# Kernel tuning notes

Measured on AMD Instinct MI355X. Metric: run time of the kernel, lower is better.

Reference implementation:

```python
import jax, jax.numpy as jnp
import numpy as np

B, S, D, H = 4, 2048, 1024, 16
HD = D // H


def sinusoidal_pe(max_len, d_model):
    pos = np.arange(max_len)[:, None].astype(np.float32)
    div = np.exp(np.arange(0, d_model, 2).astype(np.float32) * (-np.log(10000.0) / d_model))
    pe = np.zeros((max_len, d_model), dtype=np.float32)
    pe[:, 0::2] = np.sin(pos * div)
    pe[:, 1::2] = np.cos(pos * div)
    return jnp.asarray(pe)


def setup_inputs() -> dict:
    key = jax.random.key(0)
    ks = jax.random.split(key, 9)
    s = 1.0 / np.sqrt(D)
    inp = {
        "x": jax.random.normal(ks[0], (B, S, D), dtype=jnp.float32),
        "Wq": jax.random.normal(ks[1], (D, D), dtype=jnp.float32) * s,
        "bq": jnp.zeros((D,), dtype=jnp.float32),
        "Wk": jax.random.normal(ks[2], (D, D), dtype=jnp.float32) * s,
        "bk": jnp.zeros((D,), dtype=jnp.float32),
        "Wv": jax.random.normal(ks[3], (D, D), dtype=jnp.float32) * s,
        "bv": jnp.zeros((D,), dtype=jnp.float32),
        "Wp": jax.random.normal(ks[4], (D, D), dtype=jnp.float32) * s,
        "bp": jnp.zeros((D,), dtype=jnp.float32),
        "pe": sinusoidal_pe(S, D),
    }
    return inp


def reference(x, Wq, bq, Wk, bk, Wv, bv, Wp, bp, pe):
    # positional encoding (eval mode: dropout is identity)
    xp = x + pe[None, :, :]  # [B,S,D]
    split = lambda t: t.reshape(B, S, H, HD).transpose(0, 2, 1, 3)  # [B,H,S,HD]
    q = split(xp @ Wq.T + bq)
    k = split(xp @ Wk.T + bk)
    v = split(xp @ Wv.T + bv)
    scores = jnp.einsum("bhqd,bhkd->bhqk", q, k) / jnp.sqrt(jnp.float32(HD))
    attn = jax.nn.softmax(scores, axis=-1)
    ctx = jnp.einsum("bhqk,bhkd->bhqd", attn, v)
    ctx = ctx.transpose(0, 2, 1, 3).reshape(B, S, D)
    return ctx @ Wp.T + bp
```

## Files before the change

### kernel.cpp

```cpp
#include <hip/hip_runtime.h>
#include <hip/hip_bf16.h>
#include <stdint.h>

#define B_  4
#define S_  2048
#define D_  1024
#define H_  16
#define HD_ 64

typedef __bf16 bfx8   __attribute__((ext_vector_type(8)));
typedef float  f32x4  __attribute__((ext_vector_type(4)));
typedef float  f32x16 __attribute__((ext_vector_type(16)));
typedef short  s16x4  __attribute__((ext_vector_type(4)));
typedef float  fl4    __attribute__((ext_vector_type(4)));
typedef unsigned int u32x2 __attribute__((ext_vector_type(2)));
typedef unsigned int u32x4 __attribute__((ext_vector_type(4)));

#define EXP2(x) __builtin_amdgcn_exp2f(x)

static __device__ __forceinline__ unsigned short f2bf(float f) {
    union { float f; unsigned int u; } v; v.f = f;
    unsigned int r = v.u + 0x7fffu + ((v.u >> 16) & 1u);
    return (unsigned short)(r >> 16);
}
static __device__ __forceinline__ unsigned int fbits(float f) {
    union { float f; unsigned int u; } v; v.f = f; return v.u;
}

#define GLD_LDS16(gp, lp) __builtin_amdgcn_global_load_lds( \
    (const __attribute__((address_space(1))) unsigned int*)(gp), \
    (__attribute__((address_space(3))) unsigned int*)(lp), 16, 0, 0)

__global__ __launch_bounds__(256) void prep_kernel(
    const float* __restrict__ x, const float* __restrict__ pe,
    const float* __restrict__ w0, const float* __restrict__ w1,
    const float* __restrict__ w2, const float* __restrict__ w3,
    unsigned short* __restrict__ xpb, unsigned short* __restrict__ wcat)
{
    const int blk = blockIdx.x;
    if (blk < 8192) {
        int i = (blk * 256 + threadIdx.x) * 4;
        fl4 xv = *(const fl4*)(x + i);
        fl4 pv = *(const fl4*)(pe + (i & (S_ * D_ - 1)));
        s16x4 r;
#pragma unroll
        for (int j = 0; j < 4; j++) r[j] = (short)f2bf(xv[j] + pv[j]);
        *(s16x4*)(xpb + i) = r;
    } else {
        const int bb = blk - 8192;
        const int wsel = bb >> 10;
        const float* src = wsel == 0 ? w0 : wsel == 1 ? w1 : wsel == 2 ? w2 : w3;
        int i = (((bb & 1023) * 256) + threadIdx.x) * 4;
        fl4 v = *(const fl4*)(src + i);
        s16x4 r;
#pragma unroll
        for (int j = 0; j < 4; j++) r[j] = (short)f2bf(v[j]);
        *(s16x4*)(wcat + (size_t)wsel * D_ * D_ + i) = r;
    }
}

__global__ __launch_bounds__(256, 3) void gemm_qkv(
    const unsigned short* __restrict__ A,
    const unsigned short* __restrict__ Bw,
    const float* __restrict__ bq, const float* __restrict__ bk,
    const float* __restrict__ bv,
    unsigned short* __restrict__ Qo, unsigned short* __restrict__ Ko,
    unsigned short* __restrict__ Vo, float qscale)
{
    constexpr int K = D_;
    __shared__ unsigned short As[2][128 * 32];
    __shared__ unsigned short Bs[2][128 * 32];
    const int hw  = blockIdx.x;
    const int xcd = hw & 7;
    const int i_  = hw >> 3;
    const int m0  = (i_ / 3) * 128;
    const int n0  = (xcd * 3 + i_ % 3) * 128;

    const int t  = threadIdx.x;
    const int l  = t & 63;
    const int w  = t >> 6;
    const int wr = (w >> 1) * 64;
    const int wc = (w & 1) * 64;
    const int lr = l & 15;
    const int lg = l >> 4;
    const int lk = lg * 8;

    const int e0 = t * 8;
    const int sr = e0 >> 5;
    const int sc = e0 & 31;
    const unsigned short* pA = A  + (size_t)(m0 + sr) * K + sc;
    const unsigned short* pB = Bw + (size_t)(n0 + sr) * K + sc;

    f32x4 acc[4][4] = {};

    GLD_LDS16(pA,                    As[0] + e0);
    GLD_LDS16(pA + (size_t)64 * K,   As[0] + 2048 + e0);
    GLD_LDS16(pB,                    Bs[0] + e0);
    GLD_LDS16(pB + (size_t)64 * K,   Bs[0] + 2048 + e0);
    __syncthreads();

    int cur = 0;
    for (int k0 = 0; k0 < K; k0 += 32) {
        if (k0 + 32 < K) {
            GLD_LDS16(pA + k0 + 32,                    As[cur ^ 1] + e0);
            GLD_LDS16(pA + k0 + 32 + (size_t)64 * K,   As[cur ^ 1] + 2048 + e0);
            GLD_LDS16(pB + k0 + 32,                    Bs[cur ^ 1] + e0);
            GLD_LDS16(pB + k0 + 32 + (size_t)64 * K,   Bs[cur ^ 1] + 2048 + e0);
        }
        const unsigned short* Ac = As[cur];
        const unsigned short* Bc = Bs[cur];
        bfx8 af[4], bf[4];
#pragma unroll
        for (int i = 0; i < 4; i++)
            af[i] = *(const bfx8*)(Ac + (wr + i * 16 + lr) * 32 + lk);
#pragma unroll
        for (int i = 0; i < 4; i++)
            bf[i] = *(const bfx8*)(Bc + (wc + i * 16 + lr) * 32 + lk);
#pragma unroll
        for (int i = 0; i < 4; i++)
#pragma unroll
            for (int j = 0; j < 4; j++)
                acc[i][j] = __builtin_amdgcn_mfma_f32_16x16x32_bf16(
                    af[i], bf[j], acc[i][j], 0, 0, 0);
        __syncthreads();
        cur ^= 1;
    }

    const int sel = n0 >> 10;
    const float* bias = sel == 0 ? bq : sel == 1 ? bk : bv;
    const float osc = sel == 0 ? qscale : 1.0f;

#pragma unroll
    for (int i = 0; i < 4; i++) {
        const int row0 = m0 + wr + i * 16 + lg * 4;
#pragma unroll
        for (int j = 0; j < 4; j++) {
            const int colf = n0 + wc + j * 16 + lr;
            const int ocol = colf & 1023;
            const float bvv = bias[ocol];
            if (sel < 2) {
                unsigned short* C = sel == 0 ? Qo : Ko;
#pragma unroll
                for (int v = 0; v < 4; v++)
                    C[(size_t)(row0 + v) * D_ + ocol] = f2bf((acc[i][j][v] + bvv) * osc);
            } else {
                const int bidx = row0 >> 11;
                const int s0   = row0 & (S_ - 1);
                s16x4 r;
#pragma unroll
                for (int v = 0; v < 4; v++) r[v] = (short)f2bf(acc[i][j][v] + bvv);
                *(s16x4*)(Vo + (size_t)(bidx * D_ + ocol) * S_ + s0) = r;
            }
        }
    }
}

__global__ __launch_bounds__(256, 3) void gemm_out(
    const unsigned short* __restrict__ A,
    const unsigned short* __restrict__ Bw,
    const float* __restrict__ bias,
    float* __restrict__ Cout)
{
    constexpr int K = D_;
    constexpr int N = D_;
    __shared__ unsigned short As[2][128 * 32];
    __shared__ unsigned short Bs[2][128 * 32];
    const int hw = blockIdx.x;
    const int logical = (hw & 7) * 64 + (hw >> 3);
    const int m0 = (logical >> 3) * 128;
    const int n0 = (logical & 7) * 128;

    const int t  = threadIdx.x;
    const int l  = t & 63;
    const int w  = t >> 6;
    const int wr = (w >> 1) * 64;
    const int wc = (w & 1) * 64;
    const int lr = l & 15;
    const int lg = l >> 4;
    const int lk = lg * 8;

    const int e0 = t * 8;
    const int sr = e0 >> 5;
    const int sc = e0 & 31;
    const unsigned short* pA = A  + (size_t)(m0 + sr) * K + sc;
    const unsigned short* pB = Bw + (size_t)(n0 + sr) * K + sc;

    f32x4 acc[4][4] = {};

    GLD_LDS16(pA,                    As[0] + e0);
    GLD_LDS16(pA + (size_t)64 * K,   As[0] + 2048 + e0);
    GLD_LDS16(pB,                    Bs[0] + e0);
    GLD_LDS16(pB + (size_t)64 * K,   Bs[0] + 2048 + e0);
    __syncthreads();

    int cur = 0;
    for (int k0 = 0; k0 < K; k0 += 32) {
        if (k0 + 32 < K) {
            GLD_LDS16(pA + k0 + 32,                    As[cur ^ 1] + e0);
            GLD_LDS16(pA + k0 + 32 + (size_t)64 * K,   As[cur ^ 1] + 2048 + e0);
            GLD_LDS16(pB + k0 + 32,                    Bs[cur ^ 1] + e0);
            GLD_LDS16(pB + k0 + 32 + (size_t)64 * K,   Bs[cur ^ 1] + 2048 + e0);
        }
        const unsigned short* Ac = As[cur];
        const unsigned short* Bc = Bs[cur];
        bfx8 af[4], bf[4];
#pragma unroll
        for (int i = 0; i < 4; i++)
            af[i] = *(const bfx8*)(Ac + (wr + i * 16 + lr) * 32 + lk);
#pragma unroll
        for (int i = 0; i < 4; i++)
            bf[i] = *(const bfx8*)(Bc + (wc + i * 16 + lr) * 32 + lk);
#pragma unroll
        for (int i = 0; i < 4; i++)
#pragma unroll
            for (int j = 0; j < 4; j++)
                acc[i][j] = __builtin_amdgcn_mfma_f32_16x16x32_bf16(
                    af[i], bf[j], acc[i][j], 0, 0, 0);
        __syncthreads();
        cur ^= 1;
    }

#pragma unroll
    for (int i = 0; i < 4; i++) {
        const int row0 = m0 + wr + i * 16 + lg * 4;
#pragma unroll
        for (int j = 0; j < 4; j++) {
            const int col = n0 + wc + j * 16 + lr;
            const float bv = bias[col];
#pragma unroll
            for (int v = 0; v < 4; v++)
                Cout[(size_t)(row0 + v) * N + col] = acc[i][j][v] + bv;
        }
    }
}

__global__ __launch_bounds__(256, 4) void attn_kernel(
    const unsigned short* __restrict__ Qb,
    const unsigned short* __restrict__ Kb,
    const unsigned short* __restrict__ Vt,
    unsigned short* __restrict__ Ctx)
{
    __shared__ __align__(16) unsigned short Ks[2][32 * 128];
    __shared__ __align__(16) unsigned short Vs[2][32 * 128];

    const int hw = blockIdx.x;
    const int logical = (hw & 7) * 128 + (hw >> 3);
    const int bh = logical >> 4;
    const int t  = threadIdx.x;
    const int l  = t & 63;
    const int w  = t >> 6;
    const int b  = bh >> 4;
    const int h  = bh & 15;
    const int lr = l & 31;
    const int hi = l >> 5;
    const int q0 = (logical & 15) * 128 + w * 32;

    const unsigned short* Qbase = Qb + (size_t)b * S_ * D_ + h * HD_;
    const unsigned short* Kbase = Kb + (size_t)b * S_ * D_ + h * HD_;
    const unsigned short* Vbase = Vt + (size_t)bh * HD_ * S_;

    const int jrow = t >> 4;
    const int c16  = (t & 15) ^ jrow;
    const int r0   = jrow + 32 * (c16 >> 3);
    const int cc8  = (c16 & 7) * 8;
    const unsigned short* Ksrc0 = Kbase + (size_t)r0 * D_ + cc8;
    const unsigned short* Ksrc1 = Kbase + (size_t)(r0 + 16) * D_ + cc8;
    const unsigned short* Vsrc0 = Vbase + (size_t)r0 * S_ + cc8;
    const unsigned short* Vsrc1 = Vbase + (size_t)(r0 + 16) * S_ + cc8;
    const int ld0 = t * 8, ld1 = t * 8 + 2048;

    GLD_LDS16(Ksrc0, &Ks[0][ld0]);
    GLD_LDS16(Ksrc1, &Ks[0][ld1]);
    GLD_LDS16(Vsrc0, &Vs[0][ld0]);
    GLD_LDS16(Vsrc1, &Vs[0][ld1]);

    bfx8 qf[4];
#pragma unroll
    for (int t4 = 0; t4 < 4; t4++)
        qf[t4] = *(const bfx8*)(Qbase + (size_t)(q0 + lr) * D_ + t4 * 16 + hi * 8);

    f32x16 acc0 = {}, acc1 = {};
    float l_r = 0.f;
    const int sw16 = lr & 15;

#define FRD(buf, half, cs) \
    (*(const bfx8*)((buf) + lr * 128 + ((((half) * 8 + (cs)) ^ sw16) * 8)))

    int cur = 0;
    for (int ki = 0; ki < S_ / 64; ki++) {
        __syncthreads();
        if (ki + 1 < S_ / 64) {
            GLD_LDS16(Ksrc0 + (size_t)(ki + 1) * 64 * D_, &Ks[cur ^ 1][ld0]);
            GLD_LDS16(Ksrc1 + (size_t)(ki + 1) * 64 * D_, &Ks[cur ^ 1][ld1]);
            GLD_LDS16(Vsrc0 + (ki + 1) * 64,              &Vs[cur ^ 1][ld0]);
            GLD_LDS16(Vsrc1 + (ki + 1) * 64,              &Vs[cur ^ 1][ld1]);
        }
        const unsigned short* Kc = Ks[cur];
        const unsigned short* Vc = Vs[cur];

        f32x16 s0 = {}, s1 = {};
        __builtin_amdgcn_s_setprio(1);
#pragma unroll
        for (int t4 = 0; t4 < 4; t4++) {
            bfx8 a0 = FRD(Kc, 0, t4 * 2 + hi);
            bfx8 a1 = FRD(Kc, 1, t4 * 2 + hi);
            s0 = __builtin_amdgcn_mfma_f32_32x32x16_bf16(a0, qf[t4], s0, 0, 0, 0);
            s1 = __builtin_amdgcn_mfma_f32_32x32x16_bf16(a1, qf[t4], s1, 0, 0, 0);
        }
        __builtin_amdgcn_s_setprio(0);

        float c0 = 0.f, c1 = 0.f, c2 = 0.f, c3 = 0.f;
#pragma unroll
        for (int r = 0; r < 16; r += 4) {
            float p0 = EXP2(s0[r]);     s0[r] = p0;     c0 += p0;
            float p1 = EXP2(s0[r + 1]); s0[r + 1] = p1; c1 += p1;
            float p2 = EXP2(s0[r + 2]); s0[r + 2] = p2; c2 += p2;
            float p3 = EXP2(s0[r + 3]); s0[r + 3] = p3; c3 += p3;
        }
#pragma unroll
        for (int r = 0; r < 16; r += 4) {
            float p0 = EXP2(s1[r]);     s1[r] = p0;     c0 += p0;
            float p1 = EXP2(s1[r + 1]); s1[r + 1] = p1; c1 += p1;
            float p2 = EXP2(s1[r + 2]); s1[r + 2] = p2; c2 += p2;
            float p3 = EXP2(s1[r + 3]); s1[r + 3] = p3; c3 += p3;
        }
        l_r += (c0 + c1) + (c2 + c3);

        unsigned pk0[8], pk1[8];
#pragma unroll
        for (int i = 0; i < 8; i++) {
            pk0[i] = __builtin_amdgcn_perm(fbits(s0[2 * i + 1]), fbits(s0[2 * i]), 0x07060302u);
            pk1[i] = __builtin_amdgcn_perm(fbits(s1[2 * i + 1]), fbits(s1[2 * i]), 0x07060302u);
        }

#pragma unroll
        for (int ks = 0; ks < 4; ks++) {
            const int c = (ks & 1) * 4;
            const unsigned pa0 = (ks >> 1) ? pk1[c]     : pk0[c];
            const unsigned pa1 = (ks >> 1) ? pk1[c + 1] : pk0[c + 1];
            const unsigned pa2 = (ks >> 1) ? pk1[c + 2] : pk0[c + 2];
            const unsigned pa3 = (ks >> 1) ? pk1[c + 3] : pk0[c + 3];
            u32x2 r02 = __builtin_amdgcn_permlane32_swap(pa0, pa2, false, false);
            u32x2 r13 = __builtin_amdgcn_permlane32_swap(pa1, pa3, false, false);
            u32x4 bfr;
            bfr[0] = r02[0];
            bfr[1] = r13[0];
            bfr[2] = r02[1];
            bfr[3] = r13[1];
            union { u32x4 u; bfx8 b; } cvt; cvt.u = bfr;

            bfx8 v0 = FRD(Vc, 0, ks * 2 + hi);
            bfx8 v1 = FRD(Vc, 1, ks * 2 + hi);
            __builtin_amdgcn_s_setprio(1);
            acc0 = __builtin_amdgcn_mfma_f32_32x32x16_bf16(v0, cvt.b, acc0, 0, 0, 0);
            acc1 = __builtin_amdgcn_mfma_f32_32x32x16_bf16(v1, cvt.b, acc1, 0, 0, 0);
            __builtin_amdgcn_s_setprio(0);
        }
        cur ^= 1;
    }
#undef FRD

    const float l_tot = l_r + __shfl_xor(l_r, 32);
    const float rinv = 1.0f / l_tot;
    unsigned short* Cb = Ctx + (size_t)b * S_ * D_ + (size_t)(q0 + lr) * D_ + h * HD_;
#pragma unroll
    for (int dt = 0; dt < 2; dt++)
#pragma unroll
        for (int a = 0; a < 4; a++) {
            s16x4 rv;
#pragma unroll
            for (int v = 0; v < 4; v++)
                rv[v] = (short)f2bf((dt ? acc1[4 * a + v] : acc0[4 * a + v]) * rinv);
            *(s16x4*)(Cb + dt * 32 + 8 * a + 4 * hi) = rv;
        }
}

extern "C" void kernel_launch(void* const* d_in, const int* in_sizes, int n_in,
                              void* d_out, int out_size, void* d_ws, size_t ws_size,
                              hipStream_t stream)
{
    const float* x  = (const float*)d_in[0];
    const float* Wq = (const float*)d_in[1];
    const float* bq = (const float*)d_in[2];
    const float* Wk = (const float*)d_in[3];
    const float* bk = (const float*)d_in[4];
    const float* Wv = (const float*)d_in[5];
    const float* bv = (const float*)d_in[6];
    const float* Wp = (const float*)d_in[7];
    const float* bp = (const float*)d_in[8];
    const float* pe = (const float*)d_in[9];

    char* ws = (char*)d_ws;
    const size_t MD = (size_t)B_ * S_ * D_;
    unsigned short* xpb = (unsigned short*)ws; ws += MD * 2;
    unsigned short* wqb = (unsigned short*)ws; ws += (size_t)D_ * D_ * 2;
    unsigned short* wkb = (unsigned short*)ws; ws += (size_t)D_ * D_ * 2;
    unsigned short* wvb = (unsigned short*)ws; ws += (size_t)D_ * D_ * 2;
    unsigned short* wpb = (unsigned short*)ws; ws += (size_t)D_ * D_ * 2;
    unsigned short* qb  = (unsigned short*)ws; ws += MD * 2;
    unsigned short* kb  = (unsigned short*)ws; ws += MD * 2;
    unsigned short* vtb = (unsigned short*)ws; ws += MD * 2;
    unsigned short* ctb = (unsigned short*)ws; ws += MD * 2;

    prep_kernel<<<12288, 256, 0, stream>>>(x, pe, Wq, Wk, Wv, Wp, xpb, wqb);

    const float qscale = 0.125f * 1.44269504088896340736f;

    gemm_qkv<<<1536, 256, 0, stream>>>(xpb, wqb, bq, bk, bv, qb, kb, vtb, qscale);

    attn_kernel<<<1024, 256, 0, stream>>>(qb, kb, vtb, ctb);

    gemm_out<<<512, 256, 0, stream>>>(ctb, wpb, bp, (float*)d_out);
}
```

Measured before the change: 202.1 us.

## Use BK=64 XOR-swizzled LDS tiles in QKV and output GEMMs

Both projection GEMMs now stage 64-wide K slices instead of 32, which halves the number of barriers and loop iterations per tile. The LDS layout is XOR-swizzled by row so the 16-byte fragment reads avoid bank conflicts. This doubles LDS use per block, so launch bounds drop from 3 to 2 blocks per CU, giving up some occupancy in exchange for fewer syncs and conflict-free reads.

Measured after the change: 188.4 us. 6.8% less time.

```diff
diff --git a/kernel.cpp b/kernel.cpp
--- a/kernel.cpp
+++ b/kernel.cpp
@@ -59,7 +59,10 @@
     }
 }
 
-__global__ __launch_bounds__(256, 3) void gemm_qkv(
+#define RD64(buf, row, ks, lg) \
+    (*(const bfx8*)((buf) + (row) * 64 + ((((ks) * 4 + (lg)) ^ ((row) & 7)) * 8)))
+
+__global__ __launch_bounds__(256, 2) void gemm_qkv(
     const unsigned short* __restrict__ A,
     const unsigned short* __restrict__ Bw,
     const float* __restrict__ bq, const float* __restrict__ bk,
@@ -68,8 +71,8 @@
     unsigned short* __restrict__ Vo, float qscale)
 {
     constexpr int K = D_;
-    __shared__ unsigned short As[2][128 * 32];
-    __shared__ unsigned short Bs[2][128 * 32];
+    __shared__ __align__(16) unsigned short As[2][128 * 64];
+    __shared__ __align__(16) unsigned short Bs[2][128 * 64];
     const int hw  = blockIdx.x;
     const int xcd = hw & 7;
     const int i_  = hw >> 3;
@@ -83,45 +86,50 @@
     const int wc = (w & 1) * 64;
     const int lr = l & 15;
     const int lg = l >> 4;
-    const int lk = lg * 8;
-
-    const int e0 = t * 8;
-    const int sr = e0 >> 5;
-    const int sc = e0 & 31;
+
+    const int sr = t >> 3;
+    const int sc = (((t & 7) ^ (sr & 7)) * 8);
     const unsigned short* pA = A  + (size_t)(m0 + sr) * K + sc;
     const unsigned short* pB = Bw + (size_t)(n0 + sr) * K + sc;
+    const int e0 = t * 8;
+
+#define STAGE64(dst, p, kofs) do {                                   \
+    GLD_LDS16((p) + (kofs),                        (dst) + e0);      \
+    GLD_LDS16((p) + (kofs) + (size_t)32 * K,       (dst) + 2048 + e0); \
+    GLD_LDS16((p) + (kofs) + (size_t)64 * K,       (dst) + 4096 + e0); \
+    GLD_LDS16((p) + (kofs) + (size_t)96 * K,       (dst) + 6144 + e0); \
+} while (0)
 
     f32x4 acc[4][4] = {};
 
-    GLD_LDS16(pA,                    As[0] + e0);
-    GLD_LDS16(pA + (size_t)64 * K,   As[0] + 2048 + e0);
-    GLD_LDS16(pB,                    Bs[0] + e0);
-    GLD_LDS16(pB + (size_t)64 * K,   Bs[0] + 2048 + e0);
+    STAGE64(As[0], pA, 0);
+    STAGE64(Bs[0], pB, 0);
     __syncthreads();
 
     int cur = 0;
-    for (int k0 = 0; k0 < K; k0 += 32) {
-        if (k0 + 32 < K) {
-            GLD_LDS16(pA + k0 + 32,                    As[cur ^ 1] + e0);
-            GLD_LDS16(pA + k0 + 32 + (size_t)64 * K,   As[cur ^ 1] + 2048 + e0);
-            GLD_LDS16(pB + k0 + 32,                    Bs[cur ^ 1] + e0);
-            GLD_LDS16(pB + k0 + 32 + (size_t)64 * K,   Bs[cur ^ 1] + 2048 + e0);
+    for (int k0 = 0; k0 < K; k0 += 64) {
+        if (k0 + 64 < K) {
+            STAGE64(As[cur ^ 1], pA, k0 + 64);
+            STAGE64(Bs[cur ^ 1], pB, k0 + 64);
         }
         const unsigned short* Ac = As[cur];
         const unsigned short* Bc = Bs[cur];
-        bfx8 af[4], bf[4];
-#pragma unroll
-        for (int i = 0; i < 4; i++)
-            af[i] = *(const bfx8*)(Ac + (wr + i * 16 + lr) * 32 + lk);
-#pragma unroll
-        for (int i = 0; i < 4; i++)
-            bf[i] = *(const bfx8*)(Bc + (wc + i * 16 + lr) * 32 + lk);
-#pragma unroll
-        for (int i = 0; i < 4; i++)
-#pragma unroll
-            for (int j = 0; j < 4; j++)
-                acc[i][j] = __builtin_amdgcn_mfma_f32_16x16x32_bf16(
-                    af[i], bf[j], acc[i][j], 0, 0, 0);
+#pragma unroll
+        for (int ks = 0; ks < 2; ks++) {
+            bfx8 af[4], bf[4];
+#pragma unroll
+            for (int i = 0; i < 4; i++)
+                af[i] = RD64(Ac, wr + i * 16 + lr, ks, lg);
+#pragma unroll
+            for (int i = 0; i < 4; i++)
+                bf[i] = RD64(Bc, wc + i * 16 + lr, ks, lg);
+#pragma unroll
+            for (int i = 0; i < 4; i++)
+#pragma unroll
+                for (int j = 0; j < 4; j++)
+                    acc[i][j] = __builtin_amdgcn_mfma_f32_16x16x32_bf16(
+                        af[i], bf[j], acc[i][j], 0, 0, 0);
+        }
         __syncthreads();
         cur ^= 1;
     }
@@ -153,9 +161,10 @@
             }
         }
     }
-}
-
-__global__ __launch_bounds__(256, 3) void gemm_out(
+#undef STAGE64
+}
+
+__global__ __launch_bounds__(256, 2) void gemm_out(
     const unsigned short* __restrict__ A,
     const unsigned short* __restrict__ Bw,
     const float* __restrict__ bias,
@@ -163,8 +172,8 @@
 {
     constexpr int K = D_;
     constexpr int N = D_;
-    __shared__ unsigned short As[2][128 * 32];
-    __shared__ unsigned short Bs[2][128 * 32];
+    __shared__ __align__(16) unsigned short As[2][128 * 64];
+    __shared__ __align__(16) unsigned short Bs[2][128 * 64];
     const int hw = blockIdx.x;
     const int logical = (hw & 7) * 64 + (hw >> 3);
     const int m0 = (logical >> 3) * 128;
@@ -177,45 +186,50 @@
     const int wc = (w & 1) * 64;
     const int lr = l & 15;
     const int lg = l >> 4;
-    const int lk = lg * 8;
-
-    const int e0 = t * 8;
-    const int sr = e0 >> 5;
-    const int sc = e0 & 31;
+
+    const int sr = t >> 3;
+    const int sc = (((t & 7) ^ (sr & 7)) * 8);
     const unsigned short* pA = A  + (size_t)(m0 + sr) * K + sc;
     const unsigned short* pB = Bw + (size_t)(n0 + sr) * K + sc;
+    const int e0 = t * 8;
+
+#define STAGE64(dst, p, kofs) do {                                   \
+    GLD_LDS16((p) + (kofs),                        (dst) + e0);      \
+    GLD_LDS16((p) + (kofs) + (size_t)32 * K,       (dst) + 2048 + e0); \
+    GLD_LDS16((p) + (kofs) + (size_t)64 * K,       (dst) + 4096 + e0); \
+    GLD_LDS16((p) + (kofs) + (size_t)96 * K,       (dst) + 6144 + e0); \
+} while (0)
 
     f32x4 acc[4][4] = {};
 
-    GLD_LDS16(pA,                    As[0] + e0);
-    GLD_LDS16(pA + (size_t)64 * K,   As[0] + 2048 + e0);
-    GLD_LDS16(pB,                    Bs[0] + e0);
-    GLD_LDS16(pB + (size_t)64 * K,   Bs[0] + 2048 + e0);
+    STAGE64(As[0], pA, 0);
+    STAGE64(Bs[0], pB, 0);
     __syncthreads();
 
     int cur = 0;
-    for (int k0 = 0; k0 < K; k0 += 32) {
-        if (k0 + 32 < K) {
-            GLD_LDS16(pA + k0 + 32,                    As[cur ^ 1] + e0);
-            GLD_LDS16(pA + k0 + 32 + (size_t)64 * K,   As[cur ^ 1] + 2048 + e0);
-            GLD_LDS16(pB + k0 + 32,                    Bs[cur ^ 1] + e0);
-            GLD_LDS16(pB + k0 + 32 + (size_t)64 * K,   Bs[cur ^ 1] + 2048 + e0);
+    for (int k0 = 0; k0 < K; k0 += 64) {
+        if (k0 + 64 < K) {
+            STAGE64(As[cur ^ 1], pA, k0 + 64);
+            STAGE64(Bs[cur ^ 1], pB, k0 + 64);
         }
         const unsigned short* Ac = As[cur];
         const unsigned short* Bc = Bs[cur];
-        bfx8 af[4], bf[4];
-#pragma unroll
-        for (int i = 0; i < 4; i++)
-            af[i] = *(const bfx8*)(Ac + (wr + i * 16 + lr) * 32 + lk);
-#pragma unroll
-        for (int i = 0; i < 4; i++)
-            bf[i] = *(const bfx8*)(Bc + (wc + i * 16 + lr) * 32 + lk);
-#pragma unroll
-        for (int i = 0; i < 4; i++)
-#pragma unroll
-            for (int j = 0; j < 4; j++)
-                acc[i][j] = __builtin_amdgcn_mfma_f32_16x16x32_bf16(
-                    af[i], bf[j], acc[i][j], 0, 0, 0);
+#pragma unroll
+        for (int ks = 0; ks < 2; ks++) {
+            bfx8 af[4], bf[4];
+#pragma unroll
+            for (int i = 0; i < 4; i++)
+                af[i] = RD64(Ac, wr + i * 16 + lr, ks, lg);
+#pragma unroll
+            for (int i = 0; i < 4; i++)
+                bf[i] = RD64(Bc, wc + i * 16 + lr, ks, lg);
+#pragma unroll
+            for (int i = 0; i < 4; i++)
+#pragma unroll
+                for (int j = 0; j < 4; j++)
+                    acc[i][j] = __builtin_amdgcn_mfma_f32_16x16x32_bf16(
+                        af[i], bf[j], acc[i][j], 0, 0, 0);
+        }
         __syncthreads();
         cur ^= 1;
     }
@@ -232,6 +246,7 @@
                 Cout[(size_t)(row0 + v) * N + col] = acc[i][j][v] + bv;
         }
     }
+#undef STAGE64
 }
 
 __global__ __launch_bounds__(256, 4) void attn_kernel(
```
